# Kernel tuning notes

Measured on AMD Instinct MI355X. Metric: run time of the kernel, lower is better.

The kernel has to match this reference:

```python
import jax, jax.numpy as jnp
import numpy as np

C = 1.0
MIN_NORM = 1e-15
BALL_EPS = 4e-3  # hgcn eps for float32 in proj

def _norm(v):
    return jnp.maximum(jnp.linalg.norm(v, axis=-1, keepdims=True), MIN_NORM)

def artanh(y):
    return jnp.arctanh(jnp.clip(y, -1.0 + 1e-7, 1.0 - 1e-7))

def logmap0(p, c):
    sqrt_c = c ** 0.5
    pn = _norm(p)
    return p / (sqrt_c * pn) * artanh(sqrt_c * pn)

def expmap0(u, c):
    sqrt_c = c ** 0.5
    un = _norm(u)
    return jnp.tanh(sqrt_c * un) * u / (sqrt_c * un)

def proj(x, c):
    xn = _norm(x)
    maxnorm = (1.0 - BALL_EPS) / (c ** 0.5)
    return jnp.where(xn > maxnorm, x / xn * maxnorm, x)

def setup_inputs() -> dict:
    key = jax.random.key(0)
    k1, k2, k3, k4 = jax.random.split(key, 4)
    N, E, F = 100000, 640000, 128
    # points inside the Poincare ball
    x = 0.01 * jax.random.normal(k1, (N, F), dtype=jnp.float32)
    adj = jax.random.randint(k2, (2, E), 0, N, dtype=jnp.int64)
    edge_attr = jax.random.normal(k3, (E, F), dtype=jnp.float32)
    att_w = jax.random.normal(k4, (1, 3 * F), dtype=jnp.float32) * (1.0 / np.sqrt(3 * F))
    att_b = jnp.zeros((1,), dtype=jnp.float32)
    return {"x": x, "adj": adj, "edge_attr": edge_attr, "att_w": att_w, "att_b": att_b}

def reference(x, adj, edge_attr, att_w, att_b):
    N = x.shape[0]
    src, dst = adj[0], adj[1]  # agg_direction='in' -> i = 0
    xt = logmap0(x, C)  # [N, F] tangent features
    xs = xt[src]        # [E, F] gathered neighbor tangent feats
    # DenseAtt: sigmoid(Linear(cat(x_i, x_j, edge_attr)))
    feats = jnp.concatenate([xs, xt[dst], edge_attr], axis=-1)  # [E, 3F]
    adj_att = jax.nn.sigmoid(feats @ att_w.T + att_b)           # [E, 1]
    ones = jnp.ones((src.shape[0], 1), dtype=xt.dtype)
    agg_add = jax.ops.segment_sum(xs * adj_att, src, num_segments=N)
    cnt_src = jnp.maximum(jax.ops.segment_sum(ones, src, num_segments=N), 1.0)
    cnt_dst = jnp.maximum(jax.ops.segment_sum(ones, dst, num_segments=N), 1.0)
    mean_src = jax.ops.segment_sum(edge_attr, src, num_segments=N) / cnt_src
    mean_dst = jax.ops.segment_sum(edge_attr, dst, num_segments=N) / cnt_dst
    support_t = xt + agg_add + mean_src + mean_dst
    return proj(expmap0(support_t, C), C)
```

## Files before the change

kernel.cpp:

```cpp
#include <hip/hip_runtime.h>
#include <math.h>

#define F 128
#define WAVE 64
#define CAP 64

__global__ void k_zero(int* __restrict__ p, int n) {
    int i = blockIdx.x * blockDim.x + threadIdx.x;
    if (i < n) p[i] = 0;
}

__device__ __forceinline__ float halfwave_reduce_sum(float v) {
#pragma unroll
    for (int off = 16; off >= 1; off >>= 1)
        v += __shfl_xor(v, off, 64);
    return v;
}

__global__ void k_logmap(const float* __restrict__ x, const float* __restrict__ w,
                         float* __restrict__ xt, float* __restrict__ a_s,
                         float* __restrict__ a_d, int N) {
    int row = blockIdx.x * (blockDim.x >> 5) + (threadIdx.x >> 5);
    int fl = threadIdx.x & 31;
    if (row >= N) return;
    float4 v = ((const float4*)(x + (size_t)row * F))[fl];
    float ss = halfwave_reduce_sum(v.x * v.x + v.y * v.y + v.z * v.z + v.w * v.w);
    float pn = fmaxf(sqrtf(ss), 1e-15f);
    float y = fminf(pn, 1.0f - 1e-7f);
    float at = 0.5f * logf((1.0f + y) / (1.0f - y));
    float s = at / pn;
    float4 o = make_float4(v.x * s, v.y * s, v.z * s, v.w * s);
    ((float4*)(xt + (size_t)row * F))[fl] = o;
    float4 W0 = ((const float4*)w)[fl];
    float4 W1 = ((const float4*)(w + F))[fl];
    float d0 = halfwave_reduce_sum(o.x * W0.x + o.y * W0.y + o.z * W0.z + o.w * W0.w);
    float d1 = halfwave_reduce_sum(o.x * W1.x + o.y * W1.y + o.z * W1.z + o.w * W1.w);
    if (fl == 0) { a_s[row] = d0; a_d[row] = d1; }
}

__global__ void k_edge(const int* __restrict__ src, const int* __restrict__ dst,
                       const float* __restrict__ eattr, const float* __restrict__ w,
                       const float* __restrict__ bptr,
                       const float* __restrict__ a_s, const float* __restrict__ a_d,
                       int* __restrict__ cur_src, int* __restrict__ cur_dst,
                       int* __restrict__ elist_src, int* __restrict__ elist_dst,
                       float* __restrict__ S_att, int E) {
    __shared__ float dea_s[64];
    int eb = blockIdx.x * 64;
    int hw = threadIdx.x >> 5;
    int fl = threadIdx.x & 31;
    float4 W2 = ((const float4*)(w + 2 * F))[fl];
#pragma unroll
    for (int j = 0; j < 8; ++j) {
        int l = j * 8 + hw;
        int e = eb + l;
        if (e < E) {
            float4 v = ((const float4*)(eattr + (size_t)e * F))[fl];
            float p = halfwave_reduce_sum(v.x * W2.x + v.y * W2.y + v.z * W2.z + v.w * W2.w);
            if (fl == 0) dea_s[l] = p;
        }
    }
    __syncthreads();
    int tid = threadIdx.x;
    if (tid < 64) {
        int e = eb + tid;
        if (e < E) {
            int s = src[e], d = dst[e];
            float tot = a_s[s] + a_d[d] + dea_s[tid] + bptr[0];
            float att = 1.0f / (1.0f + expf(-tot));
            atomicAdd(&S_att[s], att);
            int ps = atomicAdd(&cur_src[s], 1);
            if (ps < CAP) elist_src[(size_t)s * CAP + ps] = e;
            int pd = atomicAdd(&cur_dst[d], 1);
            if (pd < CAP) elist_dst[(size_t)d * CAP + pd] = e;
        }
    }
}

__global__ void k_aggfinal(const float* __restrict__ xt, const float* __restrict__ eattr,
                           const int* __restrict__ cur_src, const int* __restrict__ cur_dst,
                           const int* __restrict__ elist_src, const int* __restrict__ elist_dst,
                           const float* __restrict__ S_att,
                           float* __restrict__ out, int N) {
    int n = blockIdx.x * (blockDim.x / WAVE) + (threadIdx.x / WAVE);
    int lane = threadIdx.x & (WAVE - 1);
    if (n >= N) return;
    int half = lane >> 5;
    int fl   = lane & 31;

    int cS = cur_src[n]; int degS = cS < CAP ? cS : CAP;
    int cD = cur_dst[n]; int degD = cD < CAP ? cD : CAP;
    int e_lnS = (lane < degS) ? elist_src[(size_t)n * CAP + lane] : 0;
    int e_lnD = (lane < degD) ? elist_dst[(size_t)n * CAP + lane] : 0;

    float4 accS = make_float4(0.f, 0.f, 0.f, 0.f);
    float4 accD = make_float4(0.f, 0.f, 0.f, 0.f);
    int degM = degS > degD ? degS : degD;
    for (int i = 0; i < degM; i += 2) {
        int idx = i + half;
        int eS = __shfl(e_lnS, idx, 64);
        int eD = __shfl(e_lnD, idx, 64);
        if (idx < degS) {
            float4 v = ((const float4*)(eattr + (size_t)eS * F))[fl];
            accS.x += v.x; accS.y += v.y; accS.z += v.z; accS.w += v.w;
        }
        if (idx < degD) {
            float4 v = ((const float4*)(eattr + (size_t)eD * F))[fl];
            accD.x += v.x; accD.y += v.y; accD.z += v.z; accD.w += v.w;
        }
    }
    accS.x += __shfl_xor(accS.x, 32, 64); accS.y += __shfl_xor(accS.y, 32, 64);
    accS.z += __shfl_xor(accS.z, 32, 64); accS.w += __shfl_xor(accS.w, 32, 64);
    accD.x += __shfl_xor(accD.x, 32, 64); accD.y += __shfl_xor(accD.y, 32, 64);
    accD.z += __shfl_xor(accD.z, 32, 64); accD.w += __shfl_xor(accD.w, 32, 64);

    float invS = 1.0f / fmaxf((float)cS, 1.0f);
    float invD = 1.0f / fmaxf((float)cD, 1.0f);
    float fa = 1.0f + S_att[n];
    float4 xv = ((const float4*)(xt + (size_t)n * F))[fl];
    float4 u;
    u.x = xv.x * fa + accS.x * invS + accD.x * invD;
    u.y = xv.y * fa + accS.y * invS + accD.y * invD;
    u.z = xv.z * fa + accS.z * invS + accD.z * invD;
    u.w = xv.w * fa + accS.w * invS + accD.w * invD;
    float pp = u.x * u.x + u.y * u.y + u.z * u.z + u.w * u.w;
#pragma unroll
    for (int off = 32; off >= 1; off >>= 1)
        pp += __shfl_xor(pp, off, 64);
    float ss = pp * 0.5f;
    float un = fmaxf(sqrtf(ss), 1e-15f);
    float t = tanhf(un);
    float scale = fminf(t, 1.0f - 4e-3f) / un;
    if (half == 0) {
        float4 o = make_float4(u.x * scale, u.y * scale, u.z * scale, u.w * scale);
        ((float4*)(out + (size_t)n * F))[fl] = o;
    }
}

extern "C" void kernel_launch(void* const* d_in, const int* in_sizes, int n_in,
                              void* d_out, int out_size, void* d_ws, size_t ws_size,
                              hipStream_t stream) {
    const float* x      = (const float*)d_in[0];
    const int*   adj    = (const int*)d_in[1];
    const float* eattr  = (const float*)d_in[2];
    const float* att_w  = (const float*)d_in[3];
    const float* att_b  = (const float*)d_in[4];
    float* out = (float*)d_out;

    const int N = in_sizes[0] / F;
    const int E = in_sizes[1] / 2;
    const int* src = adj;
    const int* dst = adj + E;

    char* ws = (char*)d_ws;
    size_t off = 0;
    float* xt        = (float*)(ws + off); off += (size_t)N * F * sizeof(float);
    float* a_s       = (float*)(ws + off); off += (size_t)N * sizeof(float);
    float* a_d       = (float*)(ws + off); off += (size_t)N * sizeof(float);
    int*   elist_src = (int*)  (ws + off); off += (size_t)N * CAP * sizeof(int);
    int*   elist_dst = (int*)  (ws + off); off += (size_t)N * CAP * sizeof(int);
    int*   zblock    = (int*)  (ws + off);
    int*   cur_src   = zblock;
    int*   cur_dst   = zblock + N;
    float* S_att     = (float*)(zblock + 2 * N);

    dim3 blk(256);
    const int RPB = 256 / WAVE;
    const int HPB = 256 / 32;

    k_zero    <<<(3 * N + 255) / 256, blk, 0, stream>>>(zblock, 3 * N);
    k_logmap  <<<(N + HPB - 1) / HPB, blk, 0, stream>>>(x, att_w, xt, a_s, a_d, N);
    k_edge    <<<(E + 63) / 64, blk, 0, stream>>>(src, dst, eattr, att_w, att_b,
                a_s, a_d, cur_src, cur_dst, elist_src, elist_dst, S_att, E);
    k_aggfinal<<<(N + RPB - 1) / RPB, blk, 0, stream>>>(xt, eattr,
                cur_src, cur_dst, elist_src, elist_dst, S_att, out, N);
}
```

Before: 267.9 us.

## Fuse attention computation into per-node aggregation and drop xt materialization

Moves the per-edge attention logit (edge_attr·w2 dot product and sigmoid) out of the edge kernel and into the node aggregation loop, where the edge_attr row is already loaded for the source mean. The edge kernel becomes a plain CSR-style fill with no full streaming read of edge_attr. The S_att float atomics disappear. The tangent features xt are no longer written out; logmap0 is recomputed from x in the final kernel. The cost is an extra gather of dst and a_d per source edge, plus a half-wave reduction inside the loop.

```diff
diff --git a/kernel.cpp b/kernel.cpp
--- a/kernel.cpp
+++ b/kernel.cpp
@@ -17,9 +17,8 @@
     return v;
 }
 
-__global__ void k_logmap(const float* __restrict__ x, const float* __restrict__ w,
-                         float* __restrict__ xt, float* __restrict__ a_s,
-                         float* __restrict__ a_d, int N) {
+__global__ void k_prenode(const float* __restrict__ x, const float* __restrict__ w,
+                          float* __restrict__ a_s, float* __restrict__ a_d, int N) {
     int row = blockIdx.x * (blockDim.x >> 5) + (threadIdx.x >> 5);
     int fl = threadIdx.x & 31;
     if (row >= N) return;
@@ -30,7 +29,6 @@
     float at = 0.5f * logf((1.0f + y) / (1.0f - y));
     float s = at / pn;
     float4 o = make_float4(v.x * s, v.y * s, v.z * s, v.w * s);
-    ((float4*)(xt + (size_t)row * F))[fl] = o;
     float4 W0 = ((const float4*)w)[fl];
     float4 W1 = ((const float4*)(w + F))[fl];
     float d0 = halfwave_reduce_sum(o.x * W0.x + o.y * W0.y + o.z * W0.z + o.w * W0.w);
@@ -38,49 +36,24 @@
     if (fl == 0) { a_s[row] = d0; a_d[row] = d1; }
 }
 
-__global__ void k_edge(const int* __restrict__ src, const int* __restrict__ dst,
-                       const float* __restrict__ eattr, const float* __restrict__ w,
-                       const float* __restrict__ bptr,
-                       const float* __restrict__ a_s, const float* __restrict__ a_d,
+__global__ void k_fill(const int* __restrict__ src, const int* __restrict__ dst,
                        int* __restrict__ cur_src, int* __restrict__ cur_dst,
-                       int* __restrict__ elist_src, int* __restrict__ elist_dst,
-                       float* __restrict__ S_att, int E) {
-    __shared__ float dea_s[64];
-    int eb = blockIdx.x * 64;
-    int hw = threadIdx.x >> 5;
-    int fl = threadIdx.x & 31;
-    float4 W2 = ((const float4*)(w + 2 * F))[fl];
-#pragma unroll
-    for (int j = 0; j < 8; ++j) {
-        int l = j * 8 + hw;
-        int e = eb + l;
-        if (e < E) {
-            float4 v = ((const float4*)(eattr + (size_t)e * F))[fl];
-            float p = halfwave_reduce_sum(v.x * W2.x + v.y * W2.y + v.z * W2.z + v.w * W2.w);
-            if (fl == 0) dea_s[l] = p;
-        }
-    }
-    __syncthreads();
-    int tid = threadIdx.x;
-    if (tid < 64) {
-        int e = eb + tid;
-        if (e < E) {
-            int s = src[e], d = dst[e];
-            float tot = a_s[s] + a_d[d] + dea_s[tid] + bptr[0];
-            float att = 1.0f / (1.0f + expf(-tot));
-            atomicAdd(&S_att[s], att);
-            int ps = atomicAdd(&cur_src[s], 1);
-            if (ps < CAP) elist_src[(size_t)s * CAP + ps] = e;
-            int pd = atomicAdd(&cur_dst[d], 1);
-            if (pd < CAP) elist_dst[(size_t)d * CAP + pd] = e;
-        }
-    }
+                       int* __restrict__ elist_src, int* __restrict__ elist_dst, int E) {
+    int e = blockIdx.x * blockDim.x + threadIdx.x;
+    if (e >= E) return;
+    int s = src[e], d = dst[e];
+    int ps = atomicAdd(&cur_src[s], 1);
+    if (ps < CAP) elist_src[(size_t)s * CAP + ps] = e;
+    int pd = atomicAdd(&cur_dst[d], 1);
+    if (pd < CAP) elist_dst[(size_t)d * CAP + pd] = e;
 }
 
-__global__ void k_aggfinal(const float* __restrict__ xt, const float* __restrict__ eattr,
+__global__ void k_aggfinal(const float* __restrict__ x, const float* __restrict__ eattr,
+                           const int* __restrict__ dst,
                            const int* __restrict__ cur_src, const int* __restrict__ cur_dst,
                            const int* __restrict__ elist_src, const int* __restrict__ elist_dst,
-                           const float* __restrict__ S_att,
+                           const float* __restrict__ a_s, const float* __restrict__ a_d,
+                           const float* __restrict__ w, const float* __restrict__ bptr,
                            float* __restrict__ out, int N) {
     int n = blockIdx.x * (blockDim.x / WAVE) + (threadIdx.x / WAVE);
     int lane = threadIdx.x & (WAVE - 1);
@@ -92,43 +65,58 @@
     int cD = cur_dst[n]; int degD = cD < CAP ? cD : CAP;
     int e_lnS = (lane < degS) ? elist_src[(size_t)n * CAP + lane] : 0;
     int e_lnD = (lane < degD) ? elist_dst[(size_t)n * CAP + lane] : 0;
+    int dstv  = (lane < degS) ? dst[e_lnS] : 0;
+    float advl = (lane < degS) ? a_d[dstv] : 0.f;
+
+    float4 W2 = ((const float4*)(w + 2 * F))[fl];
+    float a_sn = a_s[n];
+    float bias = bptr[0];
 
     float4 accS = make_float4(0.f, 0.f, 0.f, 0.f);
     float4 accD = make_float4(0.f, 0.f, 0.f, 0.f);
+    float attsum = 0.f;
     int degM = degS > degD ? degS : degD;
     for (int i = 0; i < degM; i += 2) {
         int idx = i + half;
         int eS = __shfl(e_lnS, idx, 64);
         int eD = __shfl(e_lnD, idx, 64);
+        float adv = __shfl(advl, idx, 64);
+        if (idx < degD) {
+            float4 v = ((const float4*)(eattr + (size_t)eD * F))[fl];
+            accD.x += v.x; accD.y += v.y; accD.z += v.z; accD.w += v.w;
+        }
         if (idx < degS) {
             float4 v = ((const float4*)(eattr + (size_t)eS * F))[fl];
             accS.x += v.x; accS.y += v.y; accS.z += v.z; accS.w += v.w;
-        }
-        if (idx < degD) {
-            float4 v = ((const float4*)(eattr + (size_t)eD * F))[fl];
-            accD.x += v.x; accD.y += v.y; accD.z += v.z; accD.w += v.w;
+            float p = halfwave_reduce_sum(v.x * W2.x + v.y * W2.y + v.z * W2.z + v.w * W2.w);
+            float tot = a_sn + adv + p + bias;
+            attsum += 1.0f / (1.0f + expf(-tot));
         }
     }
     accS.x += __shfl_xor(accS.x, 32, 64); accS.y += __shfl_xor(accS.y, 32, 64);
     accS.z += __shfl_xor(accS.z, 32, 64); accS.w += __shfl_xor(accS.w, 32, 64);
     accD.x += __shfl_xor(accD.x, 32, 64); accD.y += __shfl_xor(accD.y, 32, 64);
     accD.z += __shfl_xor(accD.z, 32, 64); accD.w += __shfl_xor(accD.w, 32, 64);
+    attsum += __shfl_xor(attsum, 32, 64);
+
+    float4 xv = ((const float4*)(x + (size_t)n * F))[fl];
+    float ssx = halfwave_reduce_sum(xv.x * xv.x + xv.y * xv.y + xv.z * xv.z + xv.w * xv.w);
+    float pnx = fmaxf(sqrtf(ssx), 1e-15f);
+    float yx = fminf(pnx, 1.0f - 1e-7f);
+    float atx = 0.5f * logf((1.0f + yx) / (1.0f - yx));
+    float sx = atx / pnx;
 
     float invS = 1.0f / fmaxf((float)cS, 1.0f);
     float invD = 1.0f / fmaxf((float)cD, 1.0f);
-    float fa = 1.0f + S_att[n];
-    float4 xv = ((const float4*)(xt + (size_t)n * F))[fl];
+    float fa = (1.0f + attsum) * sx;
     float4 u;
     u.x = xv.x * fa + accS.x * invS + accD.x * invD;
     u.y = xv.y * fa + accS.y * invS + accD.y * invD;
     u.z = xv.z * fa + accS.z * invS + accD.z * invD;
     u.w = xv.w * fa + accS.w * invS + accD.w * invD;
-    float pp = u.x * u.x + u.y * u.y + u.z * u.z + u.w * u.w;
-#pragma unroll
-    for (int off = 32; off >= 1; off >>= 1)
-        pp += __shfl_xor(pp, off, 64);
-    float ss = pp * 0.5f;
-    float un = fmaxf(sqrtf(ss), 1e-15f);
+
+    float pp = halfwave_reduce_sum(u.x * u.x + u.y * u.y + u.z * u.z + u.w * u.w);
+    float un = fmaxf(sqrtf(pp), 1e-15f);
     float t = tanhf(un);
     float scale = fminf(t, 1.0f - 4e-3f) / un;
     if (half == 0) {
@@ -154,7 +142,6 @@
 
     char* ws = (char*)d_ws;
     size_t off = 0;
-    float* xt        = (float*)(ws + off); off += (size_t)N * F * sizeof(float);
     float* a_s       = (float*)(ws + off); off += (size_t)N * sizeof(float);
     float* a_d       = (float*)(ws + off); off += (size_t)N * sizeof(float);
     int*   elist_src = (int*)  (ws + off); off += (size_t)N * CAP * sizeof(int);
@@ -162,16 +149,15 @@
     int*   zblock    = (int*)  (ws + off);
     int*   cur_src   = zblock;
     int*   cur_dst   = zblock + N;
-    float* S_att     = (float*)(zblock + 2 * N);
 
     dim3 blk(256);
     const int RPB = 256 / WAVE;
     const int HPB = 256 / 32;
 
-    k_zero    <<<(3 * N + 255) / 256, blk, 0, stream>>>(zblock, 3 * N);
-    k_logmap  <<<(N + HPB - 1) / HPB, blk, 0, stream>>>(x, att_w, xt, a_s, a_d, N);
-    k_edge    <<<(E + 63) / 64, blk, 0, stream>>>(src, dst, eattr, att_w, att_b,
-                a_s, a_d, cur_src, cur_dst, elist_src, elist_dst, S_att, E);
-    k_aggfinal<<<(N + RPB - 1) / RPB, blk, 0, stream>>>(xt, eattr,
-                cur_src, cur_dst, elist_src, elist_dst, S_att, out, N);
+    k_zero    <<<(2 * N + 255) / 256, blk, 0, stream>>>(zblock, 2 * N);
+    k_prenode <<<(N + HPB - 1) / HPB, blk, 0, stream>>>(x, att_w, a_s, a_d, N);
+    k_fill    <<<(E + 255) / 256, blk, 0, stream>>>(src, dst, cur_src, cur_dst,
+                                                    elist_src, elist_dst, E);
+    k_aggfinal<<<(N + RPB - 1) / RPB, blk, 0, stream>>>(x, eattr, dst,
+                cur_src, cur_dst, elist_src, elist_dst, a_s, a_d, att_w, att_b, out, N);
 }
```

After: 274.6 us. +2.5%, slower.
